# Kernel tuning notes

Hardware: AMD Instinct MI355X
Metric: run time of the kernel (lower is better)

The kernel has to match this reference:

```python
import jax, jax.numpy as jnp
import numpy as np

N = 100_000      # nodes
E = 1_600_000    # edges (avg degree 16)
F_IN = 32        # node_feat_dim
HID = 32         # hidden_dim
OUT = 1          # out_dim


def setup_inputs() -> dict:
    key = jax.random.key(0)
    ks = jax.random.split(key, 16)
    x = jax.random.normal(ks[0], (N, F_IN), dtype=jnp.float32)
    # edge_index with no self loops (PyG ChebConv removes them anyway)
    src = jax.random.randint(ks[1], (E,), 0, N, dtype=jnp.int32)
    off = jax.random.randint(ks[2], (E,), 1, N, dtype=jnp.int32)
    dst = ((src + off) % N).astype(jnp.int32)
    edge_index = jnp.stack([src, dst])

    def glorot(k, shape, fan_in, fan_out):
        s = (2.0 / (fan_in + fan_out)) ** 0.5
        return (s * jax.random.normal(k, shape)).astype(jnp.float32)

    inp = {"x": x, "edge_index": edge_index}
    names = ["xz", "hz", "xr", "hr", "xh", "hh"]
    for i, nm in enumerate(names):
        fan = F_IN if nm[0] == "x" else HID
        inp[f"W_{nm}"] = glorot(ks[3 + i], (2, fan, HID), fan, HID)  # ChebConv K=2
        inp[f"b_{nm}"] = jnp.zeros((HID,), jnp.float32)
    inp["W_gcn"] = glorot(ks[9], (HID, HID), HID, HID)
    inp["b_gcn"] = jnp.zeros((HID,), jnp.float32)
    inp["W_lin"] = glorot(ks[10], (HID, OUT), HID, OUT)
    inp["b_lin"] = jnp.zeros((OUT,), jnp.float32)
    return inp


def _forward(x, edge_index, W_xz, b_xz, W_hz, b_hz, W_xr, b_xr, W_hr, b_hr,
             W_xh, b_xh, W_hh, b_hh, W_gcn, b_gcn, W_lin, b_lin):
    src, dst = edge_index[0], edge_index[1]
    ones = jnp.ones((src.shape[0],), x.dtype)

    def agg(w, v):  # out[i] = sum_{e: dst_e = i} w_e * v[src_e]
        return jax.ops.segment_sum(w[:, None] * v[src], dst, num_segments=N)

    # --- ChebConv (sym norm, lambda_max=2): L_hat = -D^{-1/2} A D^{-1/2} ---
    deg = jax.ops.segment_sum(ones, src, num_segments=N)
    dis = jnp.where(deg > 0, jax.lax.rsqrt(jnp.maximum(deg, 1.0)), 0.0)
    lap_w = -(dis[src] * dis[dst])

    def cheb(v, W, b):  # K=2: x @ W0 + (L_hat x) @ W1 + b
        return v @ W[0] + agg(lap_w, v) @ W[1] + b

    # --- GConvGRU single step, H0 = 0 ---
    H0 = jnp.zeros((N, HID), x.dtype)
    Z = jax.nn.sigmoid(cheb(x, W_xz, b_xz) + cheb(H0, W_hz, b_hz))
    R = jax.nn.sigmoid(cheb(x, W_xr, b_xr) + cheb(H0, W_hr, b_hr))
    Ht = jnp.tanh(cheb(x, W_xh, b_xh) + cheb(H0 * R, W_hh, b_hh))
    H = Z * H0 + (1.0 - Z) * Ht

    # --- GCNConv with added self loops (deg includes self loop) ---
    deg_g = jax.ops.segment_sum(ones, dst, num_segments=N) + 1.0
    disg = jax.lax.rsqrt(deg_g)
    gw = disg[src] * disg[dst]
    hw = H @ W_gcn
    h = agg(gw, hw) + (disg * disg)[:, None] * hw + b_gcn  # neighbors + self loop
    h = jax.nn.relu(h)

    out = h @ W_lin + b_lin
    return out.squeeze(-1)


def reference(x, edge_index, W_xz, b_xz, W_hz, b_hz, W_xr, b_xr, W_hr, b_hr,
              W_xh, b_xh, W_hh, b_hh, W_gcn, b_gcn, W_lin, b_lin):
    return _forward(x, edge_index, W_xz, b_xz, W_hz, b_hz, W_xr, b_xr, W_hr, b_hr,
                    W_xh, b_xh, W_hh, b_hh, W_gcn, b_gcn, W_lin, b_lin)
```

## Files before the change

kernel.cpp:

```cpp
#include <hip/hip_runtime.h>
#include <hip/hip_fp16.h>

#define NN 100000
#define NE 1600000
#define NB 391
#define NBLK 391
#define CHUNK 4096
#define BT 1024
#define PT 1024
#define ASTR 8192

__device__ __forceinline__ float h16lo(unsigned u) {
    return __half2float(__ushort_as_half((unsigned short)(u & 0xffffu)));
}
__device__ __forceinline__ float h16hi(unsigned u) {
    return __half2float(__ushort_as_half((unsigned short)(u >> 16)));
}
__device__ __forceinline__ unsigned short h16(float f) {
    return __half_as_ushort(__float2half(f));
}
__device__ __forceinline__ unsigned pack2h(float a, float b) {
    return (unsigned)h16(a) | ((unsigned)h16(b) << 16);
}
__device__ __forceinline__ __half2 u2h2(unsigned u) {
    union { unsigned u; __half2 h; } cv; cv.u = u; return cv.h;
}

using f16x8  = __attribute__((ext_vector_type(8)))  _Float16;
using f32x16 = __attribute__((ext_vector_type(16))) float;

__global__ __launch_bounds__(1024) void k_zero(int* __restrict__ p) {
    int i = threadIdx.x;
    if (i < 784) p[i] = 0;
}

__global__ __launch_bounds__(BT) void k_bucket(
        const int* __restrict__ src, const int* __restrict__ dst,
        int* __restrict__ cur_d, int* __restrict__ cur_s,
        unsigned* __restrict__ bkd, unsigned char* __restrict__ bks) {
    __shared__ int hd[NB], hs[NB];
    __shared__ int bd[NB], bs[NB];
    __shared__ int od[NB], os[NB];
    __shared__ int t0[512], t1[512];
    __shared__ unsigned       sortd[CHUNK];
    __shared__ unsigned short sbkt [CHUNK];
    __shared__ unsigned char  sorts[CHUNK];
    __shared__ unsigned short sbkts[CHUNK];

    int tid = threadIdx.x, blk = blockIdx.x;
    if (tid < NB) { hd[tid] = 0; hs[tid] = 0; }
    __syncthreads();

    int e0 = blk * CHUNK, ee = min(e0 + CHUNK, NE);
    int sv[4], dv[4]; bool va[4];
#pragma unroll
    for (int u = 0; u < 4; ++u) {
        int e = e0 + u * BT + tid;
        va[u] = e < ee;
        if (va[u]) {
            sv[u] = src[e]; dv[u] = dst[e];
            atomicAdd(&hd[dv[u] >> 8], 1);
            atomicAdd(&hs[sv[u] >> 8], 1);
        }
    }
    __syncthreads();

    if (tid < 512) {
        t0[tid] = tid < NB ? hd[tid] : 0;
        t1[tid] = tid < NB ? hs[tid] : 0;
    }
    __syncthreads();
    for (int off = 1; off < 512; off <<= 1) {
        int a = 0, b = 0;
        if (tid < 512 && tid >= off) { a = t0[tid - off]; b = t1[tid - off]; }
        __syncthreads();
        if (tid < 512) { t0[tid] += a; t1[tid] += b; }
        __syncthreads();
    }
    if (tid < NB) {
        int c = hd[tid], c2 = hs[tid];
        od[tid] = t0[tid] - c;
        os[tid] = t1[tid] - c2;
        bd[tid] = c  ? atomicAdd(&cur_d[tid], c)  : 0;
        bs[tid] = c2 ? atomicAdd(&cur_s[tid], c2) : 0;
        hd[tid] = od[tid];
        hs[tid] = os[tid];
    }
    __syncthreads();

#pragma unroll
    for (int u = 0; u < 4; ++u) if (va[u]) {
        int bu = dv[u] >> 8;
        int p = atomicAdd(&hd[bu], 1);
        sortd[p] = ((unsigned)(dv[u] & 255) << 17) | (unsigned)sv[u];
        sbkt[p]  = (unsigned short)bu;
        int bv = sv[u] >> 8;
        int q = atomicAdd(&hs[bv], 1);
        sorts[q] = (unsigned char)(sv[u] & 255);
        sbkts[q] = (unsigned short)bv;
    }
    __syncthreads();

    int n = ee - e0;
    for (int i = tid; i < n; i += BT) {
        int b1 = sbkt[i];
        bkd[b1 * ASTR + bd[b1] + (i - od[b1])] = sortd[i];
        int b2 = sbkts[i];
        bks[b2 * ASTR + bs[b2] + (i - os[b2])] = sorts[i];
    }
}

__global__ __launch_bounds__(PT) void k_p2(const unsigned* __restrict__ bkd,
                                           const unsigned char* __restrict__ bks,
                                           const int* __restrict__ cur_d,
                                           const int* __restrict__ cur_s,
                                           int* __restrict__ cd,
                                           int* __restrict__ start,
                                           int* __restrict__ csr_s,
                                           float* __restrict__ dis,
                                           float* __restrict__ disg) {
    __shared__ int hist[256], scn[256], hsA[256];
    __shared__ int red[PT];
    int b = blockIdx.x, tid = threadIdx.x;
    if (tid < 256) { hist[tid] = 0; hsA[tid] = 0; }
    int acc = 0;
    for (int i = tid; i < b; i += PT) acc += cur_d[i];
    red[tid] = acc;
    __syncthreads();
    for (int off = PT / 2; off > 0; off >>= 1) {
        if (tid < off) red[tid] += red[tid + off];
        __syncthreads();
    }
    int cb = red[0];

    int eb = b * ASTR, ee = eb + cur_d[b];
    for (int e = eb + tid; e < ee; e += PT)
        atomicAdd(&hist[bkd[e] >> 17], 1);
    int sb = b * ASTR, se = sb + cur_s[b];
    for (int e = sb + tid; e < se; e += PT)
        atomicAdd(&hsA[bks[e]], 1);
    __syncthreads();
    int c = (tid < 256) ? hist[tid] : 0;
    if (tid < 256) scn[tid] = c;
    __syncthreads();
    for (int off = 1; off < 256; off <<= 1) {
        int t = (tid < 256 && tid >= off) ? scn[tid - off] : 0;
        __syncthreads();
        if (tid < 256) scn[tid] += t;
        __syncthreads();
    }
    if (tid < 256) {
        int excl = scn[tid] - c;
        int node = (b << 8) + tid;
        if (node < NN) {
            cd[node] = c;
            start[node] = cb + excl;
            int oc = hsA[tid];
            dis[node]  = oc > 0 ? rsqrtf((float)oc) : 0.0f;
            disg[node] = rsqrtf((float)c + 1.0f);
        }
    }
    __syncthreads();
    if (tid < 256) hsA[tid] = cb + scn[tid] - c;
    __syncthreads();
    for (int e = eb + tid; e < ee; e += PT) {
        unsigned pk = bkd[e];
        int p = atomicAdd(&hsA[pk >> 17], 1);
        csr_s[p] = (int)(pk & 0x1FFFFu);
    }
}

__global__ __launch_bounds__(256) void k_cvt(const float* __restrict__ x,
                                             const float* __restrict__ dis,
                                             unsigned short* __restrict__ xs,
                                             const float* __restrict__ W_xz,
                                             const float* __restrict__ W_xh,
                                             const float* __restrict__ W_gcn,
                                             unsigned short* __restrict__ BzT,
                                             unsigned short* __restrict__ BhT,
                                             unsigned short* __restrict__ WgT) {
    int tid = threadIdx.x;
    int i = blockIdx.x * 256 + tid;
    if (i < NN * 32) {
        xs[i] = h16(x[i] * dis[i >> 5]);
    } else if (blockIdx.x == (NN * 32) / 256) {
        for (int idx = tid; idx < 2048; idx += 256) {
            int f = idx >> 6, k = idx & 63;
            float vz = (k < 32) ? W_xz[k * 32 + f] : W_xz[1024 + (k - 32) * 32 + f];
            float vh = (k < 32) ? W_xh[k * 32 + f] : W_xh[1024 + (k - 32) * 32 + f];
            BzT[idx] = h16(vz);
            BhT[idx] = h16(vh);
        }
        for (int idx = tid; idx < 1024; idx += 256) {
            int f = idx >> 5, k = idx & 31;
            WgT[idx] = h16(W_gcn[k * 32 + f]);
        }
    }
}

__global__ __launch_bounds__(256) void k_gath_lx(const uint2* __restrict__ xs2,
                                                 const int* __restrict__ csr_s,
                                                 const int* __restrict__ start,
                                                 const int* __restrict__ cd,
                                                 const float* __restrict__ dis,
                                                 unsigned* __restrict__ Lxh) {
    int tid = threadIdx.x;
    int node = blockIdx.x * 8 + (tid >> 5);
    int lane = tid & 31, eoff = lane >> 3, c = lane & 7;
    int st = start[node], cn = cd[node];

    float a0 = 0.f, a1 = 0.f, a2 = 0.f, a3 = 0.f;
    int j = 0;
    for (; j + 16 <= cn; j += 16) {
        int s0 = csr_s[st + j + eoff];
        int s1 = csr_s[st + j + 4 + eoff];
        int s2 = csr_s[st + j + 8 + eoff];
        int s3 = csr_s[st + j + 12 + eoff];
        uint2 v0 = xs2[s0 * 8 + c];
        uint2 v1 = xs2[s1 * 8 + c];
        uint2 v2 = xs2[s2 * 8 + c];
        uint2 v3 = xs2[s3 * 8 + c];
        __half2 p01 = u2h2(0u), p23 = u2h2(0u);
        p01 = __hadd2(p01, u2h2(v0.x));  p23 = __hadd2(p23, u2h2(v0.y));
        p01 = __hadd2(p01, u2h2(v1.x));  p23 = __hadd2(p23, u2h2(v1.y));
        p01 = __hadd2(p01, u2h2(v2.x));  p23 = __hadd2(p23, u2h2(v2.y));
        p01 = __hadd2(p01, u2h2(v3.x));  p23 = __hadd2(p23, u2h2(v3.y));
        a0 += __low2float(p01);  a1 += __high2float(p01);
        a2 += __low2float(p23);  a3 += __high2float(p23);
    }
    while (j < cn) {
        int e0 = j + eoff, e1 = j + 4 + eoff;
        int c0 = e0 < cn ? e0 : cn - 1;  float m0 = e0 < cn ? 1.0f : 0.0f;
        int c1 = e1 < cn ? e1 : cn - 1;  float m1 = e1 < cn ? 1.0f : 0.0f;
        int s0 = csr_s[st + c0], s1 = csr_s[st + c1];
        uint2 v0 = xs2[s0 * 8 + c];
        uint2 v1 = xs2[s1 * 8 + c];
        a0 = fmaf(m0, h16lo(v0.x), a0);  a1 = fmaf(m0, h16hi(v0.x), a1);
        a2 = fmaf(m0, h16lo(v0.y), a2);  a3 = fmaf(m0, h16hi(v0.y), a3);
        a0 = fmaf(m1, h16lo(v1.x), a0);  a1 = fmaf(m1, h16hi(v1.x), a1);
        a2 = fmaf(m1, h16lo(v1.y), a2);  a3 = fmaf(m1, h16hi(v1.y), a3);
        j += 8;
    }
#pragma unroll
    for (int off = 8; off < 32; off <<= 1) {
        a0 += __shfl_xor(a0, off, 32);  a1 += __shfl_xor(a1, off, 32);
        a2 += __shfl_xor(a2, off, 32);  a3 += __shfl_xor(a3, off, 32);
    }
    if (lane < 8) {
        float w = -dis[node];
        Lxh[node * 16 + 2 * lane]     = pack2h(w * a0, w * a1);
        Lxh[node * 16 + 2 * lane + 1] = pack2h(w * a2, w * a3);
    }
}

__global__ __launch_bounds__(256) void k_dmm(
        const float* __restrict__ x,
        const f16x8* __restrict__ Lxh,
        const f16x8* __restrict__ BzT,
        const f16x8* __restrict__ BhT,
        const f16x8* __restrict__ WgT,
        const float* __restrict__ b_xz, const float* __restrict__ b_hz,
        const float* __restrict__ b_xh, const float* __restrict__ b_hh,
        const float* __restrict__ disg,
        unsigned short* __restrict__ hws) {
    __shared__ unsigned short Hl[4 * 1280];
    int tid = threadIdx.x;
    int wv = blockIdx.x * 4 + (tid >> 6);
    if (wv > 3124) wv = 3124;
    int l = tid & 63, mrow = l & 31, hi = l >> 5;
    int n0 = wv * 32;
    unsigned short* Hw = Hl + (tid >> 6) * 1280;

    f32x16 accz = {}, acct = {};
    const float* xrow = x + (size_t)(n0 + mrow) * 32;
#pragma unroll
    for (int c = 0; c < 2; ++c) {
        f16x8 a;
        const float* p = xrow + c * 16 + hi * 8;
#pragma unroll
        for (int e = 0; e < 8; ++e) a[e] = (_Float16)p[e];
        accz = __builtin_amdgcn_mfma_f32_32x32x16_f16(a, BzT[mrow * 8 + c * 2 + hi], accz, 0, 0, 0);
        acct = __builtin_amdgcn_mfma_f32_32x32x16_f16(a, BhT[mrow * 8 + c * 2 + hi], acct, 0, 0, 0);
    }
    const f16x8* Lrow = Lxh + (size_t)(n0 + mrow) * 4;
#pragma unroll
    for (int c = 2; c < 4; ++c) {
        f16x8 a = Lrow[(c - 2) * 2 + hi];
        accz = __builtin_amdgcn_mfma_f32_32x32x16_f16(a, BzT[mrow * 8 + c * 2 + hi], accz, 0, 0, 0);
        acct = __builtin_amdgcn_mfma_f32_32x32x16_f16(a, BhT[mrow * 8 + c * 2 + hi], acct, 0, 0, 0);
    }
    float bz = b_xz[mrow] + b_hz[mrow];
    float bh = b_xh[mrow] + b_hh[mrow];
#pragma unroll
    for (int j = 0; j < 16; ++j) {
        float z = accz[j] + bz, t = acct[j] + bh;
        float Z = 1.0f / (1.0f + expf(-z));
        float H = (1.0f - Z) * tanhf(t);
        int r = (j & 3) + 8 * (j >> 2) + 4 * hi;
        Hw[r * 40 + mrow] = h16(H);
    }
    f32x16 acch = {};
#pragma unroll
    for (int c = 0; c < 2; ++c) {
        f16x8 hfrag = *reinterpret_cast<const f16x8*>(&Hw[mrow * 40 + c * 16 + hi * 8]);
        acch = __builtin_amdgcn_mfma_f32_32x32x16_f16(hfrag, WgT[mrow * 4 + c * 2 + hi], acch, 0, 0, 0);
    }
#pragma unroll
    for (int j = 0; j < 16; ++j) {
        int r = (j & 3) + 8 * (j >> 2) + 4 * hi;
        int node = n0 + r;
        hws[node * 32 + mrow] = h16(disg[node] * acch[j]);
    }
}

__global__ __launch_bounds__(256) void k_gath_h(const uint2* __restrict__ hws2,
                                                const int* __restrict__ csr_s,
                                                const int* __restrict__ start,
                                                const int* __restrict__ cd,
                                                const float* __restrict__ disg,
                                                const float* __restrict__ b_gcn,
                                                const float* __restrict__ W_lin,
                                                const float* __restrict__ b_lin,
                                                float* __restrict__ out) {
    int tid = threadIdx.x;
    int node = blockIdx.x * 8 + (tid >> 5);
    int lane = tid & 31, eoff = lane >> 3, c = lane & 7;
    int st = start[node], cn = cd[node];

    float a0 = 0.f, a1 = 0.f, a2 = 0.f, a3 = 0.f;
    int j = 0;
    for (; j + 16 <= cn; j += 16) {
        int s0 = csr_s[st + j + eoff];
        int s1 = csr_s[st + j + 4 + eoff];
        int s2 = csr_s[st + j + 8 + eoff];
        int s3 = csr_s[st + j + 12 + eoff];
        uint2 v0 = hws2[s0 * 8 + c];
        uint2 v1 = hws2[s1 * 8 + c];
        uint2 v2 = hws2[s2 * 8 + c];
        uint2 v3 = hws2[s3 * 8 + c];
        __half2 p01 = u2h2(0u), p23 = u2h2(0u);
        p01 = __hadd2(p01, u2h2(v0.x));  p23 = __hadd2(p23, u2h2(v0.y));
        p01 = __hadd2(p01, u2h2(v1.x));  p23 = __hadd2(p23, u2h2(v1.y));
        p01 = __hadd2(p01, u2h2(v2.x));  p23 = __hadd2(p23, u2h2(v2.y));
        p01 = __hadd2(p01, u2h2(v3.x));  p23 = __hadd2(p23, u2h2(v3.y));
        a0 += __low2float(p01);  a1 += __high2float(p01);
        a2 += __low2float(p23);  a3 += __high2float(p23);
    }
    while (j < cn) {
        int e0 = j + eoff, e1 = j + 4 + eoff;
        int c0 = e0 < cn ? e0 : cn - 1;  float m0 = e0 < cn ? 1.0f : 0.0f;
        int c1 = e1 < cn ? e1 : cn - 1;  float m1 = e1 < cn ? 1.0f : 0.0f;
        int s0 = csr_s[st + c0], s1 = csr_s[st + c1];
        uint2 v0 = hws2[s0 * 8 + c];
        uint2 v1 = hws2[s1 * 8 + c];
        a0 = fmaf(m0, h16lo(v0.x), a0);  a1 = fmaf(m0, h16hi(v0.x), a1);
        a2 = fmaf(m0, h16lo(v0.y), a2);  a3 = fmaf(m0, h16hi(v0.y), a3);
        a0 = fmaf(m1, h16lo(v1.x), a0);  a1 = fmaf(m1, h16hi(v1.x), a1);
        a2 = fmaf(m1, h16lo(v1.y), a2);  a3 = fmaf(m1, h16hi(v1.y), a3);
        j += 8;
    }
#pragma unroll
    for (int off = 8; off < 32; off <<= 1) {
        a0 += __shfl_xor(a0, off, 32);  a1 += __shfl_xor(a1, off, 32);
        a2 += __shfl_xor(a2, off, 32);  a3 += __shfl_xor(a3, off, 32);
    }
    float p = 0.0f;
    if (lane < 8) {
        uint2 sv = hws2[node * 8 + lane];
        float dg = disg[node];
        int f0 = 4 * lane;
        float h0 = dg * (a0 + h16lo(sv.x)) + b_gcn[f0];
        float h1 = dg * (a1 + h16hi(sv.x)) + b_gcn[f0 + 1];
        float h2 = dg * (a2 + h16lo(sv.y)) + b_gcn[f0 + 2];
        float h3 = dg * (a3 + h16hi(sv.y)) + b_gcn[f0 + 3];
        p = fmaxf(h0, 0.0f) * W_lin[f0]
          + fmaxf(h1, 0.0f) * W_lin[f0 + 1]
          + fmaxf(h2, 0.0f) * W_lin[f0 + 2]
          + fmaxf(h3, 0.0f) * W_lin[f0 + 3];
    }
    p += __shfl_xor(p, 1, 32);
    p += __shfl_xor(p, 2, 32);
    p += __shfl_xor(p, 4, 32);
    if (lane == 0) out[node] = p + b_lin[0];
}

extern "C" void kernel_launch(void* const* d_in, const int* in_sizes, int n_in,
                              void* d_out, int out_size, void* d_ws, size_t ws_size,
                              hipStream_t stream) {
    const float* x     = (const float*)d_in[0];
    const int*   ei    = (const int*)d_in[1];
    const int*   src   = ei;
    const int*   dst   = ei + NE;
    const float* W_xz  = (const float*)d_in[2];
    const float* b_xz  = (const float*)d_in[3];
    const float* b_hz  = (const float*)d_in[5];
    const float* W_xh  = (const float*)d_in[10];
    const float* b_xh  = (const float*)d_in[11];
    const float* b_hh  = (const float*)d_in[13];
    const float* W_gcn = (const float*)d_in[14];
    const float* b_gcn = (const float*)d_in[15];
    const float* W_lin = (const float*)d_in[16];
    const float* b_lin = (const float*)d_in[17];
    float* out = (float*)d_out;

    int* w = (int*)d_ws;
    int* cur_d = w;                       w += 392;
    int* cur_s = w;                       w += 392;
    int* cd    = w;                       w += NN;
    int* start = w;                       w += NN;
    float* dis  = (float*)w;              w += NN;
    float* disg = (float*)w;              w += NN;
    unsigned short* hws = (unsigned short*)w;  w += 16 * NN;
    unsigned* Lxh = (unsigned*)w;         w += 16 * NN;
    unsigned* bkd = (unsigned*)w;         w += NB * ASTR;
    unsigned char* bks = (unsigned char*)w; w += (NB * ASTR) / 4;
    int* csr_s = w;                       w += NE;
    unsigned short* BzT = (unsigned short*)w; w += 1024;
    unsigned short* BhT = (unsigned short*)w; w += 1024;
    unsigned short* WgT = (unsigned short*)w; w += 512;
    unsigned short* xs = (unsigned short*)bkd;

    k_zero   <<<1, 1024, 0, stream>>>(cur_d);
    k_bucket <<<NBLK, BT, 0, stream>>>(src, dst, cur_d, cur_s, bkd, bks);
    k_p2     <<<NB, PT, 0, stream>>>(bkd, bks, cur_d, cur_s,
                                     cd, start, csr_s, dis, disg);
    k_cvt    <<<(NN * 32) / 256 + 1, 256, 0, stream>>>(x, dis, xs,
                                      W_xz, W_xh, W_gcn, BzT, BhT, WgT);
    k_gath_lx<<<NN / 8, 256, 0, stream>>>((const uint2*)xs, csr_s, start, cd,
                                          dis, Lxh);
    k_dmm    <<<782, 256, 0, stream>>>(x, (const f16x8*)Lxh, (const f16x8*)BzT,
                                       (const f16x8*)BhT, (const f16x8*)WgT,
                                       b_xz, b_hz, b_xh, b_hh, disg, hws);
    k_gath_h <<<NN / 8, 256, 0, stream>>>((const uint2*)hws, csr_s, start, cd,
                                          disg, b_gcn, W_lin, b_lin, out);
}
```

Measured before the change: 120.5 us.

## Fuse Laplacian gather into the dense GRU/GCN matmul kernel via shared memory

Merges the per-node Laplacian-x gather kernel with the MFMA dense stage. Each 256-thread block first gathers 32 nodes' L_hat·x rows into shared memory, then one 64-lane wave runs the MFMA GRU and GCN weight products. This removes one launch and the global round trip of the Lx intermediate. In exchange, three quarters of each block sit idle during the matmul phase, and there is a block-wide barrier between the gather and compute phases.

```diff
diff --git a/kernel.cpp b/kernel.cpp
--- a/kernel.cpp
+++ b/kernel.cpp
@@ -198,64 +198,11 @@
     }
 }
 
-__global__ __launch_bounds__(256) void k_gath_lx(const uint2* __restrict__ xs2,
-                                                 const int* __restrict__ csr_s,
-                                                 const int* __restrict__ start,
-                                                 const int* __restrict__ cd,
-                                                 const float* __restrict__ dis,
-                                                 unsigned* __restrict__ Lxh) {
-    int tid = threadIdx.x;
-    int node = blockIdx.x * 8 + (tid >> 5);
-    int lane = tid & 31, eoff = lane >> 3, c = lane & 7;
-    int st = start[node], cn = cd[node];
-
-    float a0 = 0.f, a1 = 0.f, a2 = 0.f, a3 = 0.f;
-    int j = 0;
-    for (; j + 16 <= cn; j += 16) {
-        int s0 = csr_s[st + j + eoff];
-        int s1 = csr_s[st + j + 4 + eoff];
-        int s2 = csr_s[st + j + 8 + eoff];
-        int s3 = csr_s[st + j + 12 + eoff];
-        uint2 v0 = xs2[s0 * 8 + c];
-        uint2 v1 = xs2[s1 * 8 + c];
-        uint2 v2 = xs2[s2 * 8 + c];
-        uint2 v3 = xs2[s3 * 8 + c];
-        __half2 p01 = u2h2(0u), p23 = u2h2(0u);
-        p01 = __hadd2(p01, u2h2(v0.x));  p23 = __hadd2(p23, u2h2(v0.y));
-        p01 = __hadd2(p01, u2h2(v1.x));  p23 = __hadd2(p23, u2h2(v1.y));
-        p01 = __hadd2(p01, u2h2(v2.x));  p23 = __hadd2(p23, u2h2(v2.y));
-        p01 = __hadd2(p01, u2h2(v3.x));  p23 = __hadd2(p23, u2h2(v3.y));
-        a0 += __low2float(p01);  a1 += __high2float(p01);
-        a2 += __low2float(p23);  a3 += __high2float(p23);
-    }
-    while (j < cn) {
-        int e0 = j + eoff, e1 = j + 4 + eoff;
-        int c0 = e0 < cn ? e0 : cn - 1;  float m0 = e0 < cn ? 1.0f : 0.0f;
-        int c1 = e1 < cn ? e1 : cn - 1;  float m1 = e1 < cn ? 1.0f : 0.0f;
-        int s0 = csr_s[st + c0], s1 = csr_s[st + c1];
-        uint2 v0 = xs2[s0 * 8 + c];
-        uint2 v1 = xs2[s1 * 8 + c];
-        a0 = fmaf(m0, h16lo(v0.x), a0);  a1 = fmaf(m0, h16hi(v0.x), a1);
-        a2 = fmaf(m0, h16lo(v0.y), a2);  a3 = fmaf(m0, h16hi(v0.y), a3);
-        a0 = fmaf(m1, h16lo(v1.x), a0);  a1 = fmaf(m1, h16hi(v1.x), a1);
-        a2 = fmaf(m1, h16lo(v1.y), a2);  a3 = fmaf(m1, h16hi(v1.y), a3);
-        j += 8;
-    }
-#pragma unroll
-    for (int off = 8; off < 32; off <<= 1) {
-        a0 += __shfl_xor(a0, off, 32);  a1 += __shfl_xor(a1, off, 32);
-        a2 += __shfl_xor(a2, off, 32);  a3 += __shfl_xor(a3, off, 32);
-    }
-    if (lane < 8) {
-        float w = -dis[node];
-        Lxh[node * 16 + 2 * lane]     = pack2h(w * a0, w * a1);
-        Lxh[node * 16 + 2 * lane + 1] = pack2h(w * a2, w * a3);
-    }
-}
-
-__global__ __launch_bounds__(256) void k_dmm(
-        const float* __restrict__ x,
-        const f16x8* __restrict__ Lxh,
+__global__ __launch_bounds__(256) void k_lxdmm(
+        const uint2* __restrict__ xs2,
+        const int* __restrict__ csr_s,
+        const int* __restrict__ start, const int* __restrict__ cd,
+        const float* __restrict__ dis, const float* __restrict__ x,
         const f16x8* __restrict__ BzT,
         const f16x8* __restrict__ BhT,
         const f16x8* __restrict__ WgT,
@@ -263,31 +210,80 @@
         const float* __restrict__ b_xh, const float* __restrict__ b_hh,
         const float* __restrict__ disg,
         unsigned short* __restrict__ hws) {
-    __shared__ unsigned short Hl[4 * 1280];
-    int tid = threadIdx.x;
-    int wv = blockIdx.x * 4 + (tid >> 6);
-    if (wv > 3124) wv = 3124;
-    int l = tid & 63, mrow = l & 31, hi = l >> 5;
-    int n0 = wv * 32;
-    unsigned short* Hw = Hl + (tid >> 6) * 1280;
-
+    __shared__ __align__(16) unsigned LxL[32 * 20];
+    __shared__ __align__(16) unsigned short Hw[1280];
+    int tid = threadIdx.x, blk = blockIdx.x;
+    int n0 = blk * 32;
+    int grp = tid >> 5, lane = tid & 31, eoff = lane >> 3, c = lane & 7;
+
+#pragma unroll 1
+    for (int b = 0; b < 4; ++b) {
+        int nl = b * 8 + grp;
+        int node = n0 + nl;
+        int st = start[node], cn = cd[node];
+        float a0 = 0.f, a1 = 0.f, a2 = 0.f, a3 = 0.f;
+        int j = 0;
+        for (; j + 16 <= cn; j += 16) {
+            int s0 = csr_s[st + j + eoff];
+            int s1 = csr_s[st + j + 4 + eoff];
+            int s2 = csr_s[st + j + 8 + eoff];
+            int s3 = csr_s[st + j + 12 + eoff];
+            uint2 v0 = xs2[s0 * 8 + c];
+            uint2 v1 = xs2[s1 * 8 + c];
+            uint2 v2 = xs2[s2 * 8 + c];
+            uint2 v3 = xs2[s3 * 8 + c];
+            __half2 p01 = u2h2(0u), p23 = u2h2(0u);
+            p01 = __hadd2(p01, u2h2(v0.x));  p23 = __hadd2(p23, u2h2(v0.y));
+            p01 = __hadd2(p01, u2h2(v1.x));  p23 = __hadd2(p23, u2h2(v1.y));
+            p01 = __hadd2(p01, u2h2(v2.x));  p23 = __hadd2(p23, u2h2(v2.y));
+            p01 = __hadd2(p01, u2h2(v3.x));  p23 = __hadd2(p23, u2h2(v3.y));
+            a0 += __low2float(p01);  a1 += __high2float(p01);
+            a2 += __low2float(p23);  a3 += __high2float(p23);
+        }
+        while (j < cn) {
+            int e0 = j + eoff, e1 = j + 4 + eoff;
+            int c0 = e0 < cn ? e0 : cn - 1;  float m0 = e0 < cn ? 1.0f : 0.0f;
+            int c1 = e1 < cn ? e1 : cn - 1;  float m1 = e1 < cn ? 1.0f : 0.0f;
+            int s0 = csr_s[st + c0], s1 = csr_s[st + c1];
+            uint2 v0 = xs2[s0 * 8 + c];
+            uint2 v1 = xs2[s1 * 8 + c];
+            a0 = fmaf(m0, h16lo(v0.x), a0);  a1 = fmaf(m0, h16hi(v0.x), a1);
+            a2 = fmaf(m0, h16lo(v0.y), a2);  a3 = fmaf(m0, h16hi(v0.y), a3);
+            a0 = fmaf(m1, h16lo(v1.x), a0);  a1 = fmaf(m1, h16hi(v1.x), a1);
+            a2 = fmaf(m1, h16lo(v1.y), a2);  a3 = fmaf(m1, h16hi(v1.y), a3);
+            j += 8;
+        }
+#pragma unroll
+        for (int off = 8; off < 32; off <<= 1) {
+            a0 += __shfl_xor(a0, off, 32);  a1 += __shfl_xor(a1, off, 32);
+            a2 += __shfl_xor(a2, off, 32);  a3 += __shfl_xor(a3, off, 32);
+        }
+        if (lane < 8) {
+            float w = -dis[node];
+            LxL[nl * 20 + 2 * lane]     = pack2h(w * a0, w * a1);
+            LxL[nl * 20 + 2 * lane + 1] = pack2h(w * a2, w * a3);
+        }
+    }
+    __syncthreads();
+    if (tid >= 64) return;
+
+    int mrow = tid & 31, hi = tid >> 5;
     f32x16 accz = {}, acct = {};
     const float* xrow = x + (size_t)(n0 + mrow) * 32;
 #pragma unroll
-    for (int c = 0; c < 2; ++c) {
+    for (int cc = 0; cc < 2; ++cc) {
         f16x8 a;
-        const float* p = xrow + c * 16 + hi * 8;
+        const float* p = xrow + cc * 16 + hi * 8;
 #pragma unroll
         for (int e = 0; e < 8; ++e) a[e] = (_Float16)p[e];
-        accz = __builtin_amdgcn_mfma_f32_32x32x16_f16(a, BzT[mrow * 8 + c * 2 + hi], accz, 0, 0, 0);
-        acct = __builtin_amdgcn_mfma_f32_32x32x16_f16(a, BhT[mrow * 8 + c * 2 + hi], acct, 0, 0, 0);
-    }
-    const f16x8* Lrow = Lxh + (size_t)(n0 + mrow) * 4;
-#pragma unroll
-    for (int c = 2; c < 4; ++c) {
-        f16x8 a = Lrow[(c - 2) * 2 + hi];
-        accz = __builtin_amdgcn_mfma_f32_32x32x16_f16(a, BzT[mrow * 8 + c * 2 + hi], accz, 0, 0, 0);
-        acct = __builtin_amdgcn_mfma_f32_32x32x16_f16(a, BhT[mrow * 8 + c * 2 + hi], acct, 0, 0, 0);
+        accz = __builtin_amdgcn_mfma_f32_32x32x16_f16(a, BzT[mrow * 8 + cc * 2 + hi], accz, 0, 0, 0);
+        acct = __builtin_amdgcn_mfma_f32_32x32x16_f16(a, BhT[mrow * 8 + cc * 2 + hi], acct, 0, 0, 0);
+    }
+#pragma unroll
+    for (int cc = 2; cc < 4; ++cc) {
+        f16x8 a = *reinterpret_cast<const f16x8*>(&LxL[mrow * 20 + (cc - 2) * 8 + hi * 4]);
+        accz = __builtin_amdgcn_mfma_f32_32x32x16_f16(a, BzT[mrow * 8 + cc * 2 + hi], accz, 0, 0, 0);
+        acct = __builtin_amdgcn_mfma_f32_32x32x16_f16(a, BhT[mrow * 8 + cc * 2 + hi], acct, 0, 0, 0);
     }
     float bz = b_xz[mrow] + b_hz[mrow];
     float bh = b_xh[mrow] + b_hh[mrow];
@@ -301,9 +297,9 @@
     }
     f32x16 acch = {};
 #pragma unroll
-    for (int c = 0; c < 2; ++c) {
-        f16x8 hfrag = *reinterpret_cast<const f16x8*>(&Hw[mrow * 40 + c * 16 + hi * 8]);
-        acch = __builtin_amdgcn_mfma_f32_32x32x16_f16(hfrag, WgT[mrow * 4 + c * 2 + hi], acch, 0, 0, 0);
+    for (int cc = 0; cc < 2; ++cc) {
+        f16x8 hfrag = *reinterpret_cast<const f16x8*>(&Hw[mrow * 40 + cc * 16 + hi * 8]);
+        acch = __builtin_amdgcn_mfma_f32_32x32x16_f16(hfrag, WgT[mrow * 4 + cc * 2 + hi], acch, 0, 0, 0);
     }
 #pragma unroll
     for (int j = 0; j < 16; ++j) {
@@ -411,7 +407,6 @@
     float* dis  = (float*)w;              w += NN;
     float* disg = (float*)w;              w += NN;
     unsigned short* hws = (unsigned short*)w;  w += 16 * NN;
-    unsigned* Lxh = (unsigned*)w;         w += 16 * NN;
     unsigned* bkd = (unsigned*)w;         w += NB * ASTR;
     unsigned char* bks = (unsigned char*)w; w += (NB * ASTR) / 4;
     int* csr_s = w;                       w += NE;
@@ -426,11 +421,10 @@
                                      cd, start, csr_s, dis, disg);
     k_cvt    <<<(NN * 32) / 256 + 1, 256, 0, stream>>>(x, dis, xs,
                                       W_xz, W_xh, W_gcn, BzT, BhT, WgT);
-    k_gath_lx<<<NN / 8, 256, 0, stream>>>((const uint2*)xs, csr_s, start, cd,
-                                          dis, Lxh);
-    k_dmm    <<<782, 256, 0, stream>>>(x, (const f16x8*)Lxh, (const f16x8*)BzT,
-                                       (const f16x8*)BhT, (const f16x8*)WgT,
-                                       b_xz, b_hz, b_xh, b_hh, disg, hws);
+    k_lxdmm  <<<NN / 32, 256, 0, stream>>>((const uint2*)xs, csr_s, start, cd,
+                                           dis, x, (const f16x8*)BzT,
+                                           (const f16x8*)BhT, (const f16x8*)WgT,
+                                           b_xz, b_hz, b_xh, b_hh, disg, hws);
     k_gath_h <<<NN / 8, 256, 0, stream>>>((const uint2*)hws, csr_s, start, cd,
                                           disg, b_gcn, W_lin, b_lin, out);
 }
```

Result: slower. 126.4 us (+4.9%).
